# Kernel tuning notes

Hardware: AMD Instinct MI355X
Metric: run time of the kernel (lower is better)

The kernel has to match this reference:

```python
import jax, jax.numpy as jnp
import numpy as np

N = 50000
E = 800000
D = 128  # feature / hidden dim
NEG_SLOPE = 0.2


def gat_layer(x, src, dst, W, a_src, a_dst, b):
    """PyG-style GATConv (heads=1, add_self_loops already applied to src/dst)."""
    h = x @ W                                   # [N, D]
    s_src = h @ a_src                           # [N]
    s_dst = h @ a_dst                           # [N]
    e = jax.nn.leaky_relu(s_src[src] + s_dst[dst], NEG_SLOPE)  # [E+N]
    # softmax over incoming edges per target node (stable)
    m = jax.ops.segment_max(e, dst, num_segments=N)            # [N]
    e = jnp.exp(e - m[dst])
    denom = jax.ops.segment_sum(e, dst, num_segments=N)        # [N]
    alpha = e / denom[dst]                                     # [E+N]
    msg = h[src] * alpha[:, None]                              # [E+N, D]
    out = jax.ops.segment_sum(msg, dst, num_segments=N)        # [N, D]
    return out + b


def setup_inputs() -> dict:
    key = jax.random.key(0)
    ks = jax.random.split(key, 16)
    sc = 1.0 / np.sqrt(D)
    inp = {
        "x": jax.random.normal(ks[0], (N, D), dtype=jnp.float32),
        "edge_index": jax.random.randint(ks[1], (2, E), 0, N, dtype=jnp.int64),
        # encoder params (in=D)
        "We": jax.random.normal(ks[2], (D, D), dtype=jnp.float32) * sc,
        "ae_s": jax.random.normal(ks[3], (D,), dtype=jnp.float32) * sc,
        "ae_d": jax.random.normal(ks[4], (D,), dtype=jnp.float32) * sc,
        "be": jnp.zeros((D,), dtype=jnp.float32),
        # processor params (in=2D due to concat with encoded)
        "Wp": jax.random.normal(ks[5], (2 * D, D), dtype=jnp.float32) * sc,
        "ap_s": jax.random.normal(ks[6], (D,), dtype=jnp.float32) * sc,
        "ap_d": jax.random.normal(ks[7], (D,), dtype=jnp.float32) * sc,
        "bp": jnp.zeros((D,), dtype=jnp.float32),
        # decoder params (in=D)
        "Wd": jax.random.normal(ks[8], (D, D), dtype=jnp.float32) * sc,
        "ad_s": jax.random.normal(ks[9], (D,), dtype=jnp.float32) * sc,
        "ad_d": jax.random.normal(ks[10], (D,), dtype=jnp.float32) * sc,
        "bd": jnp.zeros((D,), dtype=jnp.float32),
    }
    return inp


def reference(x, edge_index, We, ae_s, ae_d, be, Wp, ap_s, ap_d, bp, Wd, ad_s, ad_d, bd):
    # add self-loops (GATConv default)
    loops = jnp.arange(N, dtype=edge_index.dtype)
    src = jnp.concatenate([edge_index[0], loops])
    dst = jnp.concatenate([edge_index[1], loops])

    h = gat_layer(x, src, dst, We, ae_s, ae_d, be)   # encode
    encoded = h
    for _ in range(2):                                # num_processing_steps
        h = gat_layer(jnp.concatenate([h, encoded], axis=-1), src, dst, Wp, ap_s, ap_d, bp)
    out = gat_layer(h, src, dst, Wd, ad_s, ad_d, bd)  # decode (outputer is None)
    return out
```

## Files before the change

kernel.cpp:

```cpp
#include <hip/hip_runtime.h>

#define DD 128
#define LRELU_SLOPE 0.2f
#define NPART 8
#define LOG2E 1.4426950408889634f

typedef unsigned short u16;
typedef unsigned int   u32;
typedef __attribute__((ext_vector_type(8))) short short8;
typedef __attribute__((ext_vector_type(4))) float f32x4;

__device__ __forceinline__ u16 f2bf(float f) {
    union { float f; u32 u; } v; v.f = f;
    u32 r = (v.u + 0x7fffu + ((v.u >> 16) & 1u)) >> 16;
    return (u16)r;
}
__device__ __forceinline__ float bf2f(u32 hi16) {
    union { u32 u; float f; } v; v.u = hi16 << 16;
    return v.f;
}

__global__ void detect_and_zero_kernel(const int* __restrict__ ei32, int* __restrict__ flag,
                                       int E, int* __restrict__ cnt, int N) {
    int i = blockIdx.x * blockDim.x + threadIdx.x;
    if (i < N) cnt[i] = 0;
    if (blockIdx.x == 0) {
        __shared__ int any_nz;
        if (threadIdx.x == 0) any_nz = 0;
        __syncthreads();
        int nz = 0;
        int kmax = (E < 4096) ? E : 4096;
        for (int k = threadIdx.x; k < kmax; k += blockDim.x)
            if (ei32[2 * k + 1] != 0) nz = 1;
        if (nz) atomicOr(&any_nz, 1);
        __syncthreads();
        if (threadIdx.x == 0) *flag = any_nz ? 0 : 1;
    }
}

__device__ __forceinline__ int load_dst(const void* ei, int is64, int E, int i) {
    return is64 ? (int)((const long long*)ei)[E + i] : ((const int*)ei)[E + i];
}
__device__ __forceinline__ int load_src(const void* ei, int is64, int E, int i) {
    return is64 ? (int)((const long long*)ei)[i] : ((const int*)ei)[i];
}

__global__ void scatter_slot_kernel(const void* __restrict__ ei, const int* __restrict__ flag,
                                    int* __restrict__ cnt, int* __restrict__ esrc,
                                    int E, int N, int pdiv) {
    int part = blockIdx.x & (NPART - 1);
    int i = (blockIdx.x >> 3) * blockDim.x + threadIdx.x;
    int tot = E + N;
    if (i >= tot) return;
    int f = *flag;
    int s, d;
    if (i < E) {
        d = load_dst(ei, f, E, i);
        if ((unsigned)d >= (unsigned)N || d / pdiv != part) return;
        s = load_src(ei, f, E, i);
        if ((unsigned)s >= (unsigned)N) return;
    } else {
        s = d = i - E;
        if (d / pdiv != part) return;
    }
    int pos = atomicAdd(&cnt[d], 1);
    if (pos < 64) esrc[((u32)d << 6) | pos] = s;
}

__global__ void pack_w_kernel(const float* __restrict__ We, const float* __restrict__ Wp,
                              const float* __restrict__ Wd, u16* __restrict__ Wpack) {
    int blk = blockIdx.x;
    int l = threadIdx.x;
    int panel = blk >> 5, t = (blk >> 3) & 3, c = blk & 7;
    const float* src = (panel == 0) ? We : (panel == 3) ? Wd : Wp + (size_t)(panel - 1) * 128 * DD;
    u16* dst = Wpack + ((((size_t)panel * 4 + t) * 8 + c) * 64 + l) * 8;
    int krow = t * 32 + (l >> 4) * 8;
    int col = c * 16 + (l & 15);
#pragma unroll
    for (int j = 0; j < 8; ++j)
        dst[j] = f2bf(src[(size_t)(krow + j) * DD + col]);
}

__device__ __forceinline__ short8 load_afrag(const float* p) {
    float4 a = *(const float4*)p;
    float4 b = *(const float4*)(p + 4);
    union { short8 v; u16 u[8]; } r;
    r.u[0] = f2bf(a.x); r.u[1] = f2bf(a.y); r.u[2] = f2bf(a.z); r.u[3] = f2bf(a.w);
    r.u[4] = f2bf(b.x); r.u[5] = f2bf(b.y); r.u[6] = f2bf(b.z); r.u[7] = f2bf(b.w);
    return r.v;
}
__device__ __forceinline__ short8 load_afrag(const u16* p) {
    return *(const short8*)p;
}

template <int PHASES, typename XT>
__global__ __launch_bounds__(256) void gemm_mfma_kernel(
    const XT* __restrict__ X0, const XT* __restrict__ X1,
    const u16* __restrict__ Wpack,
    const float* __restrict__ a_s, const float* __restrict__ a_d,
    u16* __restrict__ H, float* __restrict__ Ss, float* __restrict__ Sd, int N) {

    __shared__ u16 Wlds[4 * 8 * 64 * 8];
    const int tid  = threadIdx.x;
    const int lane = tid & 63;
    const int wv   = tid >> 6;

    const int rb = blockIdx.x * 64 + wv * 16;
    int lrow = rb + (lane & 15); if (lrow >= N) lrow = N - 1;
    const int koff = (lane >> 4) * 8;

    f32x4 acc[8];
#pragma unroll
    for (int c = 0; c < 8; ++c) acc[c] = (f32x4){0.f, 0.f, 0.f, 0.f};

#pragma unroll
    for (int p = 0; p < PHASES; ++p) {
        __syncthreads();
        {
            const uint4* s = (const uint4*)(Wpack + (size_t)p * 16384);
            uint4* d = (uint4*)Wlds;
            for (int i = tid; i < 2048; i += 256) d[i] = s[i];
        }
        __syncthreads();
        const XT* xrow = ((p == 0) ? X0 : X1) + (size_t)lrow * DD;
#pragma unroll
        for (int t = 0; t < 4; ++t) {
            short8 af = load_afrag(xrow + t * 32 + koff);
            const u16* wb = &Wlds[((t * 8) * 64 + lane) * 8];
#pragma unroll
            for (int c = 0; c < 8; ++c) {
                short8 bf = *(const short8*)(wb + c * 512);
                acc[c] = __builtin_amdgcn_mfma_f32_16x16x32_bf16(af, bf, acc[c], 0, 0, 0);
            }
        }
    }

    const int colb = lane & 15;
    const int r0 = rb + (lane >> 4) * 4;
    float ps[4] = {0.f, 0.f, 0.f, 0.f};
    float pd[4] = {0.f, 0.f, 0.f, 0.f};
#pragma unroll
    for (int c = 0; c < 8; ++c) {
        float as_c = a_s[c * 16 + colb];
        float ad_c = a_d[c * 16 + colb];
#pragma unroll
        for (int r = 0; r < 4; ++r) {
            float v = acc[c][r];
            ps[r] += v * as_c;
            pd[r] += v * ad_c;
            int row = r0 + r;
            if (row < N) H[(size_t)row * DD + c * 16 + colb] = f2bf(v);
        }
    }
#pragma unroll
    for (int r = 0; r < 4; ++r) {
        float s1 = ps[r], s2 = pd[r];
#pragma unroll
        for (int m = 1; m < 16; m <<= 1) {
            s1 += __shfl_xor(s1, m, 64);
            s2 += __shfl_xor(s2, m, 64);
        }
        int row = r0 + r;
        if (colb == 0 && row < N) { Ss[row] = s1 * LOG2E; Sd[row] = s2 * LOG2E; }
    }
}

__device__ __forceinline__ float lrelu(float v) {
    return fmaxf(v, LRELU_SLOPE * v);
}

template <typename OT>
__global__ __launch_bounds__(256) void gat_edge_kernel(
    const u16* __restrict__ H, const float* __restrict__ Ss, const float* __restrict__ Sd,
    const int* __restrict__ cnt, const int* __restrict__ esrc,
    const float* __restrict__ bias, OT* __restrict__ OUT, int N) {

    const int tid  = threadIdx.x;
    const int lane = tid & 63;
    const int sub  = lane >> 4;
    const int c8   = lane & 15;
    const int node = (blockIdx.x * blockDim.x + tid) >> 6;
    if (node >= N) return;

    const int beg = node << 6;
    int cv = cnt[node]; if (cv > 64) cv = 64;
    const int end = beg + cv;
    const float sd = Sd[node];
    const int last = end - 1;

    const uint4* H4 = (const uint4*)H;
    float dn = 0.f;
    float A[8];
#pragma unroll
    for (int k = 0; k < 8; ++k) A[k] = 0.f;

    for (int j = beg; j < end; j += 16) {
        int e0 = j + sub, e1 = j + 4 + sub, e2 = j + 8 + sub, e3 = j + 12 + sub;
        bool v0 = e0 < end, v1 = e1 < end, v2 = e2 < end, v3 = e3 < end;
        int s0 = esrc[v0 ? e0 : last];
        int s1 = esrc[v1 ? e1 : last];
        int s2 = esrc[v2 ? e2 : last];
        int s3 = esrc[v3 ? e3 : last];
        float c0 = Ss[(u32)s0];
        float c1 = Ss[(u32)s1];
        float c2 = Ss[(u32)s2];
        float c3 = Ss[(u32)s3];
        uint4 h0 = H4[((u32)s0 << 4) | c8];
        uint4 h1 = H4[((u32)s1 << 4) | c8];
        uint4 h2 = H4[((u32)s2 << 4) | c8];
        uint4 h3 = H4[((u32)s3 << 4) | c8];
        float p0 = v0 ? __builtin_amdgcn_exp2f(lrelu(c0 + sd)) : 0.f;
        float p1 = v1 ? __builtin_amdgcn_exp2f(lrelu(c1 + sd)) : 0.f;
        float p2 = v2 ? __builtin_amdgcn_exp2f(lrelu(c2 + sd)) : 0.f;
        float p3 = v3 ? __builtin_amdgcn_exp2f(lrelu(c3 + sd)) : 0.f;
        dn += ((p0 + p1) + (p2 + p3));
        A[0] += p0 * bf2f(h0.x & 0xffffu) + p1 * bf2f(h1.x & 0xffffu)
              + p2 * bf2f(h2.x & 0xffffu) + p3 * bf2f(h3.x & 0xffffu);
        A[1] += p0 * bf2f(h0.x >> 16)     + p1 * bf2f(h1.x >> 16)
              + p2 * bf2f(h2.x >> 16)     + p3 * bf2f(h3.x >> 16);
        A[2] += p0 * bf2f(h0.y & 0xffffu) + p1 * bf2f(h1.y & 0xffffu)
              + p2 * bf2f(h2.y & 0xffffu) + p3 * bf2f(h3.y & 0xffffu);
        A[3] += p0 * bf2f(h0.y >> 16)     + p1 * bf2f(h1.y >> 16)
              + p2 * bf2f(h2.y >> 16)     + p3 * bf2f(h3.y >> 16);
        A[4] += p0 * bf2f(h0.z & 0xffffu) + p1 * bf2f(h1.z & 0xffffu)
              + p2 * bf2f(h2.z & 0xffffu) + p3 * bf2f(h3.z & 0xffffu);
        A[5] += p0 * bf2f(h0.z >> 16)     + p1 * bf2f(h1.z >> 16)
              + p2 * bf2f(h2.z >> 16)     + p3 * bf2f(h3.z >> 16);
        A[6] += p0 * bf2f(h0.w & 0xffffu) + p1 * bf2f(h1.w & 0xffffu)
              + p2 * bf2f(h2.w & 0xffffu) + p3 * bf2f(h3.w & 0xffffu);
        A[7] += p0 * bf2f(h0.w >> 16)     + p1 * bf2f(h1.w >> 16)
              + p2 * bf2f(h2.w >> 16)     + p3 * bf2f(h3.w >> 16);
    }

    dn += __shfl_xor(dn, 16, 64);
    dn += __shfl_xor(dn, 32, 64);
#pragma unroll
    for (int k = 0; k < 8; ++k) {
        float v = A[k];
        v += __shfl_xor(v, 16, 64);
        v += __shfl_xor(v, 32, 64);
        A[k] = v;
    }

    if (sub == 0) {
        float inv = 1.f / dn;
        float4 b0 = *(const float4*)(bias + 8 * c8);
        float4 b1 = *(const float4*)(bias + 8 * c8 + 4);
        float o[8];
        o[0] = A[0] * inv + b0.x; o[1] = A[1] * inv + b0.y;
        o[2] = A[2] * inv + b0.z; o[3] = A[3] * inv + b0.w;
        o[4] = A[4] * inv + b1.x; o[5] = A[5] * inv + b1.y;
        o[6] = A[6] * inv + b1.z; o[7] = A[7] * inv + b1.w;
        if constexpr (sizeof(OT) == 2) {
            uint4 pk;
            pk.x = (u32)f2bf(o[0]) | ((u32)f2bf(o[1]) << 16);
            pk.y = (u32)f2bf(o[2]) | ((u32)f2bf(o[3]) << 16);
            pk.z = (u32)f2bf(o[4]) | ((u32)f2bf(o[5]) << 16);
            pk.w = (u32)f2bf(o[6]) | ((u32)f2bf(o[7]) << 16);
            ((uint4*)OUT)[((u32)node << 4) | c8] = pk;
        } else {
            float4* O4 = (float4*)OUT;
            O4[((u32)node << 5) | (c8 * 2)]     = make_float4(o[0], o[1], o[2], o[3]);
            O4[((u32)node << 5) | (c8 * 2 + 1)] = make_float4(o[4], o[5], o[6], o[7]);
        }
    }
}

extern "C" void kernel_launch(void* const* d_in, const int* in_sizes, int n_in,
                              void* d_out, int out_size, void* d_ws, size_t ws_size,
                              hipStream_t stream) {
    const float* x    = (const float*)d_in[0];
    const void*  ei   = d_in[1];
    const float* We   = (const float*)d_in[2];
    const float* ae_s = (const float*)d_in[3];
    const float* ae_d = (const float*)d_in[4];
    const float* be   = (const float*)d_in[5];
    const float* Wp   = (const float*)d_in[6];
    const float* ap_s = (const float*)d_in[7];
    const float* ap_d = (const float*)d_in[8];
    const float* bp   = (const float*)d_in[9];
    const float* Wd   = (const float*)d_in[10];
    const float* ad_s = (const float*)d_in[11];
    const float* ad_d = (const float*)d_in[12];
    const float* bd   = (const float*)d_in[13];

    const int N = in_sizes[0] / DD;
    const int E = in_sizes[1] / 2;
    const int ETOT = E + N;
    const int pdiv = (N + NPART - 1) / NPART;

    char* w = (char*)d_ws;
    u16*  Wpack = (u16*)w;   w += (size_t)4 * 16384 * 2;
    u16*  Hb    = (u16*)w;   w += (size_t)N * DD * 2;
    u16*  f_enc = (u16*)w;   w += (size_t)N * DD * 2;
    u16*  f_x   = (u16*)w;   w += (size_t)N * DD * 2;
    float* Ss   = (float*)w; w += (size_t)N * 4;
    float* Sd   = (float*)w; w += (size_t)N * 4;
    int*  cnt   = (int*)w;   w += (size_t)N * 4;
    int*  esrc  = (int*)w;   w += (size_t)N * 64 * 4;
    int*  flag  = (int*)w;   w += 256;
    if ((size_t)(w - (char*)d_ws) > ws_size) return;

    float* out = (float*)d_out;

    {
        int gZero = (N > 4096 ? N : 4096);
        detect_and_zero_kernel<<<(gZero + 255) / 256, 256, 0, stream>>>(
            (const int*)ei, flag, E, cnt, N);
        int gPart = ((ETOT + 255) / 256) * NPART;
        scatter_slot_kernel<<<gPart, 256, 0, stream>>>(ei, flag, cnt, esrc, E, N, pdiv);
    }

    pack_w_kernel<<<128, 64, 0, stream>>>(We, Wp, Wd, Wpack);

    const int gG = (N + 63) / 64;
    const int gE = (N + 3) / 4;

    gemm_mfma_kernel<1, float><<<gG, 256, 0, stream>>>(x, x, Wpack + 0 * 16384,
                                                       ae_s, ae_d, Hb, Ss, Sd, N);
    gat_edge_kernel<u16><<<gE, 256, 0, stream>>>(Hb, Ss, Sd, cnt, esrc, be, f_enc, N);

    gemm_mfma_kernel<2, u16><<<gG, 256, 0, stream>>>(f_enc, f_enc, Wpack + 1 * 16384,
                                                     ap_s, ap_d, Hb, Ss, Sd, N);
    gat_edge_kernel<u16><<<gE, 256, 0, stream>>>(Hb, Ss, Sd, cnt, esrc, bp, f_x, N);

    gemm_mfma_kernel<2, u16><<<gG, 256, 0, stream>>>(f_x, f_enc, Wpack + 1 * 16384,
                                                     ap_s, ap_d, Hb, Ss, Sd, N);
    gat_edge_kernel<u16><<<gE, 256, 0, stream>>>(Hb, Ss, Sd, cnt, esrc, bp, f_x, N);

    gemm_mfma_kernel<1, u16><<<gG, 256, 0, stream>>>(f_x, f_x, Wpack + 3 * 16384,
                                                     ad_s, ad_d, Hb, Ss, Sd, N);
    gat_edge_kernel<float><<<gE, 256, 0, stream>>>(Hb, Ss, Sd, cnt, esrc, bd, out, N);
}
```

Measured before the change: 232.6 us.

## Fold duplicated concat into summed weight panel and double GEMM rows per wave

For the first processor layer the input is concat(enc, enc), so the two halves of Wp are pre-summed into a fifth packed panel and that GEMM runs a single K=128 phase instead of two. Separately, each wave now computes 32 rows with two accumulator sets sharing each LDS B-fragment, halving the grid and the number of weight loads into LDS. The summed weights are rounded to bf16 after the add, which shifts rounding slightly, and the doubled accumulators raise register pressure.

```diff
diff --git a/kernel.cpp b/kernel.cpp
--- a/kernel.cpp
+++ b/kernel.cpp
@@ -72,13 +72,21 @@
     int blk = blockIdx.x;
     int l = threadIdx.x;
     int panel = blk >> 5, t = (blk >> 3) & 3, c = blk & 7;
-    const float* src = (panel == 0) ? We : (panel == 3) ? Wd : Wp + (size_t)(panel - 1) * 128 * DD;
     u16* dst = Wpack + ((((size_t)panel * 4 + t) * 8 + c) * 64 + l) * 8;
     int krow = t * 32 + (l >> 4) * 8;
     int col = c * 16 + (l & 15);
-#pragma unroll
-    for (int j = 0; j < 8; ++j)
-        dst[j] = f2bf(src[(size_t)(krow + j) * DD + col]);
+    if (panel == 4) {
+#pragma unroll
+        for (int j = 0; j < 8; ++j)
+            dst[j] = f2bf(Wp[(size_t)(krow + j) * DD + col] +
+                          Wp[(size_t)(krow + j + 128) * DD + col]);
+    } else {
+        const float* src = (panel == 0) ? We : (panel == 3) ? Wd
+                         : Wp + (size_t)(panel - 1) * 128 * DD;
+#pragma unroll
+        for (int j = 0; j < 8; ++j)
+            dst[j] = f2bf(src[(size_t)(krow + j) * DD + col]);
+    }
 }
 
 __device__ __forceinline__ short8 load_afrag(const float* p) {
@@ -105,13 +113,17 @@
     const int lane = tid & 63;
     const int wv   = tid >> 6;
 
-    const int rb = blockIdx.x * 64 + wv * 16;
-    int lrow = rb + (lane & 15); if (lrow >= N) lrow = N - 1;
+    const int rb = blockIdx.x * 128 + wv * 32;
+    int lrow0 = rb + (lane & 15);      if (lrow0 >= N) lrow0 = N - 1;
+    int lrow1 = rb + 16 + (lane & 15); if (lrow1 >= N) lrow1 = N - 1;
     const int koff = (lane >> 4) * 8;
 
-    f32x4 acc[8];
-#pragma unroll
-    for (int c = 0; c < 8; ++c) acc[c] = (f32x4){0.f, 0.f, 0.f, 0.f};
+    f32x4 acc0[8], acc1[8];
+#pragma unroll
+    for (int c = 0; c < 8; ++c) {
+        acc0[c] = (f32x4){0.f, 0.f, 0.f, 0.f};
+        acc1[c] = (f32x4){0.f, 0.f, 0.f, 0.f};
+    }
 
 #pragma unroll
     for (int p = 0; p < PHASES; ++p) {
@@ -122,46 +134,54 @@
             for (int i = tid; i < 2048; i += 256) d[i] = s[i];
         }
         __syncthreads();
-        const XT* xrow = ((p == 0) ? X0 : X1) + (size_t)lrow * DD;
+        const XT* X = (p == 0) ? X0 : X1;
+        const XT* xr0 = X + (size_t)lrow0 * DD;
+        const XT* xr1 = X + (size_t)lrow1 * DD;
 #pragma unroll
         for (int t = 0; t < 4; ++t) {
-            short8 af = load_afrag(xrow + t * 32 + koff);
+            short8 af0 = load_afrag(xr0 + t * 32 + koff);
+            short8 af1 = load_afrag(xr1 + t * 32 + koff);
             const u16* wb = &Wlds[((t * 8) * 64 + lane) * 8];
 #pragma unroll
             for (int c = 0; c < 8; ++c) {
                 short8 bf = *(const short8*)(wb + c * 512);
-                acc[c] = __builtin_amdgcn_mfma_f32_16x16x32_bf16(af, bf, acc[c], 0, 0, 0);
+                acc0[c] = __builtin_amdgcn_mfma_f32_16x16x32_bf16(af0, bf, acc0[c], 0, 0, 0);
+                acc1[c] = __builtin_amdgcn_mfma_f32_16x16x32_bf16(af1, bf, acc1[c], 0, 0, 0);
             }
         }
     }
 
     const int colb = lane & 15;
-    const int r0 = rb + (lane >> 4) * 4;
-    float ps[4] = {0.f, 0.f, 0.f, 0.f};
-    float pd[4] = {0.f, 0.f, 0.f, 0.f};
-#pragma unroll
-    for (int c = 0; c < 8; ++c) {
-        float as_c = a_s[c * 16 + colb];
-        float ad_c = a_d[c * 16 + colb];
+#pragma unroll
+    for (int g = 0; g < 2; ++g) {
+        const f32x4* acc = g ? acc1 : acc0;
+        const int r0 = rb + g * 16 + (lane >> 4) * 4;
+        float ps[4] = {0.f, 0.f, 0.f, 0.f};
+        float pd[4] = {0.f, 0.f, 0.f, 0.f};
+#pragma unroll
+        for (int c = 0; c < 8; ++c) {
+            float as_c = a_s[c * 16 + colb];
+            float ad_c = a_d[c * 16 + colb];
+#pragma unroll
+            for (int r = 0; r < 4; ++r) {
+                float v = acc[c][r];
+                ps[r] += v * as_c;
+                pd[r] += v * ad_c;
+                int row = r0 + r;
+                if (row < N) H[(size_t)row * DD + c * 16 + colb] = f2bf(v);
+            }
+        }
 #pragma unroll
         for (int r = 0; r < 4; ++r) {
-            float v = acc[c][r];
-            ps[r] += v * as_c;
-            pd[r] += v * ad_c;
+            float s1 = ps[r], s2 = pd[r];
+#pragma unroll
+            for (int m = 1; m < 16; m <<= 1) {
+                s1 += __shfl_xor(s1, m, 64);
+                s2 += __shfl_xor(s2, m, 64);
+            }
             int row = r0 + r;
-            if (row < N) H[(size_t)row * DD + c * 16 + colb] = f2bf(v);
-        }
-    }
-#pragma unroll
-    for (int r = 0; r < 4; ++r) {
-        float s1 = ps[r], s2 = pd[r];
-#pragma unroll
-        for (int m = 1; m < 16; m <<= 1) {
-            s1 += __shfl_xor(s1, m, 64);
-            s2 += __shfl_xor(s2, m, 64);
-        }
-        int row = r0 + r;
-        if (colb == 0 && row < N) { Ss[row] = s1 * LOG2E; Sd[row] = s2 * LOG2E; }
+            if (colb == 0 && row < N) { Ss[row] = s1 * LOG2E; Sd[row] = s2 * LOG2E; }
+        }
     }
 }
 
@@ -290,7 +310,7 @@
     const int pdiv = (N + NPART - 1) / NPART;
 
     char* w = (char*)d_ws;
-    u16*  Wpack = (u16*)w;   w += (size_t)4 * 16384 * 2;
+    u16*  Wpack = (u16*)w;   w += (size_t)5 * 16384 * 2;
     u16*  Hb    = (u16*)w;   w += (size_t)N * DD * 2;
     u16*  f_enc = (u16*)w;   w += (size_t)N * DD * 2;
     u16*  f_x   = (u16*)w;   w += (size_t)N * DD * 2;
@@ -311,16 +331,16 @@
         scatter_slot_kernel<<<gPart, 256, 0, stream>>>(ei, flag, cnt, esrc, E, N, pdiv);
     }
 
-    pack_w_kernel<<<128, 64, 0, stream>>>(We, Wp, Wd, Wpack);
-
-    const int gG = (N + 63) / 64;
+    pack_w_kernel<<<160, 64, 0, stream>>>(We, Wp, Wd, Wpack);
+
+    const int gG = (N + 127) / 128;
     const int gE = (N + 3) / 4;
 
     gemm_mfma_kernel<1, float><<<gG, 256, 0, stream>>>(x, x, Wpack + 0 * 16384,
                                                        ae_s, ae_d, Hb, Ss, Sd, N);
     gat_edge_kernel<u16><<<gE, 256, 0, stream>>>(Hb, Ss, Sd, cnt, esrc, be, f_enc, N);
 
-    gemm_mfma_kernel<2, u16><<<gG, 256, 0, stream>>>(f_enc, f_enc, Wpack + 1 * 16384,
+    gemm_mfma_kernel<1, u16><<<gG, 256, 0, stream>>>(f_enc, f_enc, Wpack + 4 * 16384,
                                                      ap_s, ap_d, Hb, Ss, Sd, N);
     gat_edge_kernel<u16><<<gE, 256, 0, stream>>>(Hb, Ss, Sd, cnt, esrc, bp, f_x, N);
 
```

Result: no change. 235.4 us (+1.2%).
